# Optimization experiments

Measured on AMD Instinct MI355X. Metric: run time of the kernel, lower is better.

## Reference

```python
import jax, jax.numpy as jnp
import numpy as np

# dims: B=1, T=2048 (prefill), dim=3072, Hq=32, Hkv=8, D=128, S=max_seq_len=4096

def _rotate_interleave(x):
    # (-x1, x0, -x3, x2, ...) pairwise rotation on last dim
    x = x.reshape(x.shape[:-1] + (-1, 2))
    x = jnp.stack((-x[..., 1], x[..., 0]), axis=-1)
    return x.reshape(x.shape[:-2] + (-1,))


def setup_inputs() -> dict:
    key = jax.random.key(0)
    ks = jax.random.split(key, 8)
    B, T, DIM, HQ, HKV, HD, S = 1, 2048, 3072, 32, 8, 128, 4096
    x = jax.random.normal(ks[0], (B, T, DIM), jnp.float32)
    wq = jax.random.normal(ks[1], (HQ * HD, DIM), jnp.float32) * 0.02
    wk = jax.random.normal(ks[2], (HKV * HD, DIM), jnp.float32) * 0.02
    wv = jax.random.normal(ks[3], (HKV * HD, DIM), jnp.float32) * 0.02
    wo = jax.random.normal(ks[4], (DIM, HQ * HD), jnp.float32) * 0.02
    freqs_cos = jax.random.uniform(ks[5], (T, HD), jnp.float32)
    freqs_sin = jax.random.uniform(ks[6], (T, HD), jnp.float32)
    input_pos = jnp.zeros((1,), jnp.int32)
    k_cache = jnp.zeros((1, S, HKV, HD), jnp.float32)
    v_cache = jnp.zeros((1, S, HKV, HD), jnp.float32)
    return {"x": x, "wq": wq, "wk": wk, "wv": wv, "wo": wo,
            "freqs_cos": freqs_cos, "freqs_sin": freqs_sin,
            "k_cache": k_cache, "v_cache": v_cache, "input_pos": input_pos}


def reference(x, wq, wk, wv, wo, freqs_cos, freqs_sin, k_cache, v_cache, input_pos):
    B, T, _ = x.shape
    HQ, HKV, HD = 32, 8, 128
    q = (x @ wq.T).reshape(B, T, HQ, HD)
    k = (x @ wk.T).reshape(B, T, HKV, HD)
    v = (x @ wv.T).reshape(B, T, HKV, HD)
    # interleaved RoPE (computed in fp32 as in apply_rotary_emb)
    fc = freqs_cos[None, :, None, :]
    fs = freqs_sin[None, :, None, :]
    q = q * fc + _rotate_interleave(q) * fs
    k = k * fc + _rotate_interleave(k) * fs
    # KV-cache update at start_pos (torch.ops.llama.update_cache)
    sp = input_pos[0]
    k_all = jax.lax.dynamic_update_slice(k_cache, k, (0, sp, 0, 0))  # [1,S,HKV,HD]
    v_all = jax.lax.dynamic_update_slice(v_cache, v, (0, sp, 0, 0))
    S = k_all.shape[1]
    # GQA: expand kv heads to match q heads (head h -> kv head h // rep)
    rep = HQ // HKV
    kr = jnp.repeat(k_all, rep, axis=2)  # [1,S,HQ,HD]
    vr = jnp.repeat(v_all, rep, axis=2)
    scale = 1.0 / np.sqrt(HD).astype(np.float32)
    scores = jnp.einsum('bthd,bshd->bhts', q, kr) * scale  # [B,HQ,T,S]
    # causal mask relative to start_pos (custom_sdpa is_causal=True path)
    qpos = sp + jnp.arange(T)
    kpos = jnp.arange(S)
    mask = kpos[None, :] <= qpos[:, None]                   # [T,S]
    scores = jnp.where(mask[None, None], scores, jnp.float32(-1e30))
    attn = jax.nn.softmax(scores, axis=-1)
    y = jnp.einsum('bhts,bshd->bthd', attn, vr).reshape(B, T, HQ * HD)
    return y @ wo.T
```

## Files before the change

kernel.cpp:

```cpp
#include <hip/hip_runtime.h>
#include <hip/hip_bf16.h>
#include <stdint.h>

typedef float f32x4 __attribute__((ext_vector_type(4)));
typedef short s16x8 __attribute__((ext_vector_type(8)));
typedef short s16x4 __attribute__((ext_vector_type(4)));
typedef unsigned short u16x2 __attribute__((ext_vector_type(2)));
typedef unsigned short u16x4 __attribute__((ext_vector_type(4)));

#define AS1 __attribute__((address_space(1)))
#define AS3 __attribute__((address_space(3)))

static constexpr int T_    = 2048;
static constexpr int DIM_  = 3072;
static constexpr int HQ_   = 32;
static constexpr int HKV_  = 8;
static constexpr int HD_   = 128;
static constexpr int S_    = 4096;
static constexpr int NQKV_ = HQ_ * HD_ + 2 * HKV_ * HD_;

__device__ __forceinline__ unsigned short f2b(float f) {
  return __builtin_bit_cast(unsigned short, __float2bfloat16(f));
}
__device__ __forceinline__ float b2f(unsigned short u) {
  return __bfloat162float(__builtin_bit_cast(__hip_bfloat16, u));
}
__device__ __forceinline__ float exp2a(float x) {
  float r; asm("v_exp_f32 %0, %1" : "=v"(r) : "v"(x)); return r;
}

__device__ __forceinline__ void gld_lds16(const void* g, void* l) {
  __builtin_amdgcn_global_load_lds((AS1 unsigned int*)(uintptr_t)g,
                                   (AS3 unsigned int*)l, 16, 0, 0);
}

#define FENCE() asm volatile("" ::: "memory")
#define BAR()   do { FENCE(); __builtin_amdgcn_s_barrier(); FENCE(); } while (0)
#define WAIT_VM(n)   asm volatile("s_waitcnt vmcnt(" #n ")" ::: "memory")
#define WAIT_LGKM(n) asm volatile("s_waitcnt lgkmcnt(" #n ")" ::: "memory")
#define SCHEDB()     __builtin_amdgcn_sched_barrier(0)

__global__ __launch_bounds__(256)
void k_cvt(const float* __restrict__ src, unsigned short* __restrict__ dst, int n4) {
  int i = blockIdx.x * 256 + threadIdx.x;
  if (i >= n4) return;
  float4 v = reinterpret_cast<const float4*>(src)[i];
  u16x4 o;
  o.x = f2b(v.x); o.y = f2b(v.y); o.z = f2b(v.z); o.w = f2b(v.w);
  reinterpret_cast<u16x4*>(dst)[i] = o;
}

__global__ __launch_bounds__(256)
void k_cvtW(const float* __restrict__ wq, const float* __restrict__ wk,
            const float* __restrict__ wv, unsigned short* __restrict__ dst) {
  int idx = blockIdx.x * 256 + threadIdx.x;
  if (idx >= 4718592) return;
  const float* src; int s;
  if (idx < 3145728)      { src = wq; s = idx; }
  else if (idx < 3932160) { src = wk; s = idx - 3145728; }
  else                    { src = wv; s = idx - 3932160; }
  float4 v = reinterpret_cast<const float4*>(src)[s];
  u16x4 o;
  o.x = f2b(v.x); o.y = f2b(v.y); o.z = f2b(v.z); o.w = f2b(v.w);
  reinterpret_cast<u16x4*>(dst)[idx] = o;
}

template<bool OUT_BF16>
__global__ __launch_bounds__(512, 4)
void k_gemm192(const unsigned short* __restrict__ A,
               const unsigned short* __restrict__ B,
               void* __restrict__ Cout, int N, int K, int KT,
               int nbn, int xcdq) {
  __shared__ char lds[81920];
  const int bid = blockIdx.x;
  const int swz = (bid & 7) * xcdq + (bid >> 3);
  const int bm  = swz / nbn, bn = swz % nbn;
  const int tid = threadIdx.x, lane = tid & 63, wid = tid >> 6;
  const int wm  = wid >> 2, wn = wid & 3;
  const int r16 = lane & 15, q4 = lane >> 4;

  const unsigned short* Ag = A + (size_t)(bm * 128) * K;
  const unsigned short* Bg = B + (size_t)(bn * 192) * K;

  const int srow = tid >> 3;
  const int scol = ((tid & 7) ^ (srow & 7)) * 8;

  f32x4 acc[4][3] = {};
  s16x8 af[4][2];

  auto stageA = [&](int c, int r, int t) {
    gld_lds16(Ag + (size_t)(r * 64 + srow) * K + t * 64 + scol,
              lds + c * 40960 + r * 8192 + tid * 16);
  };
  auto stageB = [&](int c, int r, int t) {
    gld_lds16(Bg + (size_t)(r * 64 + srow) * K + t * 64 + scol,
              lds + c * 40960 + 16384 + r * 8192 + tid * 16);
  };
  auto readA = [&](int c) {
    #pragma unroll
    for (int i = 0; i < 4; ++i) {
      const int arow = wm * 64 + i * 16 + r16;
      #pragma unroll
      for (int kk = 0; kk < 2; ++kk)
        af[i][kk] = *(const s16x8*)(lds + c * 40960 + arow * 128 +
                                    (((kk * 4 + q4) ^ (arow & 7)) << 4));
    }
  };
  auto readB = [&](s16x8 (&dst)[2], int c, int j) {
    const int brow = wn * 48 + j * 16 + r16;
    #pragma unroll
    for (int kk = 0; kk < 2; ++kk)
      dst[kk] = *(const s16x8*)(lds + c * 40960 + 16384 + brow * 128 +
                                (((kk * 4 + q4) ^ (brow & 7)) << 4));
  };

#define MFMA8(BF, J)                                                           \
  __builtin_amdgcn_s_setprio(1);                                               \
  _Pragma("unroll")                                                            \
  for (int i_ = 0; i_ < 4; ++i_) {                                             \
    _Pragma("unroll")                                                          \
    for (int kk_ = 0; kk_ < 2; ++kk_)                                          \
      acc[i_][J] = __builtin_amdgcn_mfma_f32_16x16x32_bf16(                    \
          af[i_][kk_], BF[kk_], acc[i_][J], 0, 0, 0);                          \
  }                                                                            \
  __builtin_amdgcn_s_setprio(0);

  stageA(0, 0, 0); stageA(0, 1, 0);
  stageB(0, 0, 0); stageB(0, 1, 0); stageB(0, 2, 0);
  WAIT_VM(0);
  BAR();

  for (int t = 0; t < KT; ++t) {
    const int c = t & 1;
    const bool hn = (t + 1 < KT);
    {
      s16x8 bfc[2];
      readA(c); readB(bfc, c, 0);
      if (hn) { stageA(c ^ 1, 0, t + 1); stageA(c ^ 1, 1, t + 1); }
      BAR();
      WAIT_LGKM(0); SCHEDB();
      MFMA8(bfc, 0);
      BAR();
    }
    {
      s16x8 bfc[2];
      readB(bfc, c, 1);
      if (hn) { stageB(c ^ 1, 0, t + 1); stageB(c ^ 1, 1, t + 1); }
      BAR();
      WAIT_LGKM(0); SCHEDB();
      MFMA8(bfc, 1);
      BAR();
    }
    {
      s16x8 bfc[2];
      readB(bfc, c, 2);
      if (hn) stageB(c ^ 1, 2, t + 1);
      BAR();
      WAIT_LGKM(0); SCHEDB();
      MFMA8(bfc, 2);
      if (hn) { WAIT_VM(0); }
      BAR();
    }
  }
#undef MFMA8

  #pragma unroll
  for (int i = 0; i < 4; ++i) {
    const int row = bm * 128 + wm * 64 + i * 16 + q4 * 4;
    #pragma unroll
    for (int j = 0; j < 3; ++j) {
      const int col = bn * 192 + wn * 48 + j * 16 + r16;
      if constexpr (OUT_BF16) {
        unsigned short* C = (unsigned short*)Cout;
        #pragma unroll
        for (int rr = 0; rr < 4; ++rr)
          C[(size_t)(row + rr) * N + col] = f2b(acc[i][j][rr]);
      } else {
        float* C = (float*)Cout;
        #pragma unroll
        for (int rr = 0; rr < 4; ++rr)
          C[(size_t)(row + rr) * N + col] = acc[i][j][rr];
      }
    }
  }
}

__global__ __launch_bounds__(256)
void k_rope_q(const unsigned short* __restrict__ qkv,
              const float* __restrict__ fc, const float* __restrict__ fs,
              unsigned short* __restrict__ Qr) {
  int idx = blockIdx.x * 256 + threadIdx.x;
  int t   = idx >> 11;
  int rem = idx & 2047;
  int h   = rem >> 6;
  int d0  = (rem & 63) << 1;
  size_t qoff = (size_t)t * NQKV_ + h * HD_ + d0;
  u16x2 xv = *reinterpret_cast<const u16x2*>(&qkv[qoff]);
  float x0 = b2f(xv.x), x1 = b2f(xv.y);
  float c0 = fc[t * HD_ + d0], c1 = fc[t * HD_ + d0 + 1];
  float s0 = fs[t * HD_ + d0], s1 = fs[t * HD_ + d0 + 1];
  u16x2 o;
  o.x = f2b(x0 * c0 - x1 * s0);
  o.y = f2b(x1 * c1 + x0 * s1);
  *reinterpret_cast<u16x2*>(&Qr[((size_t)h * T_ + t) * HD_ + d0]) = o;
}

__global__ __launch_bounds__(256)
void k_rope_k(const unsigned short* __restrict__ qkv,
              const float* __restrict__ fc, const float* __restrict__ fs,
              unsigned short* __restrict__ Kall, const int* __restrict__ ipos) {
  int idx = blockIdx.x * 256 + threadIdx.x;
  int t   = idx >> 9;
  int rem = idx & 511;
  int hk  = rem >> 6;
  int d0  = (rem & 63) << 1;
  int sp  = ipos[0];
  size_t qoff = (size_t)t * NQKV_ + HQ_ * HD_ + hk * HD_ + d0;
  u16x2 xv = *reinterpret_cast<const u16x2*>(&qkv[qoff]);
  float x0 = b2f(xv.x), x1 = b2f(xv.y);
  float c0 = fc[t * HD_ + d0], c1 = fc[t * HD_ + d0 + 1];
  float s0 = fs[t * HD_ + d0], s1 = fs[t * HD_ + d0 + 1];
  unsigned short o0 = f2b(x0 * c0 - x1 * s0);
  unsigned short o1 = f2b(x1 * c1 + x0 * s1);
  size_t ooff = ((size_t)hk * S_ + sp + t) * HD_ + d0;
  Kall[ooff] = o0; Kall[ooff + 1] = o1;
}

__global__ __launch_bounds__(256)
void k_prefix(const float* __restrict__ kc, const float* __restrict__ vc,
              unsigned short* __restrict__ Kall, unsigned short* __restrict__ VT,
              const int* __restrict__ ipos) {
  int sp = ipos[0];
  int total = sp * HKV_ * HD_;
  for (int idx = blockIdx.x * 256 + threadIdx.x; idx < total;
       idx += gridDim.x * 256) {
    int s   = idx >> 10;
    int rem = idx & 1023;
    int hk  = rem >> 7;
    int d   = rem & 127;
    Kall[((size_t)hk * S_ + s) * HD_ + d] = f2b(kc[((size_t)s * HKV_ + hk) * HD_ + d]);
    VT[((size_t)hk * HD_ + d) * S_ + s]   = f2b(vc[((size_t)s * HKV_ + hk) * HD_ + d]);
  }
}

__global__ __launch_bounds__(256)
void k_vt(const unsigned short* __restrict__ qkv,
          unsigned short* __restrict__ VT, const int* __restrict__ ipos) {
  int hk = blockIdx.x >> 5;
  int tt = blockIdx.x & 31;
  int sp = ipos[0];
  __shared__ unsigned short lds[64][136];
  int tid = threadIdx.x;
  #pragma unroll
  for (int p = 0; p < 4; ++p) {
    int e   = p * 256 + tid;
    int tr  = e >> 4;
    int col = (e & 15) << 3;
    *reinterpret_cast<s16x8*>(&lds[tr][col]) =
        *reinterpret_cast<const s16x8*>(&qkv[(size_t)(tt * 64 + tr) * NQKV_ + (HQ_ + HKV_) * HD_ + hk * HD_ + col]);
  }
  __syncthreads();
  #pragma unroll
  for (int p = 0; p < 32; ++p) {
    int e = p * 256 + tid;
    int d = e >> 6;
    int t = e & 63;
    VT[((size_t)hk * HD_ + d) * S_ + sp + tt * 64 + t] = lds[t][d];
  }
}

__global__ __launch_bounds__(256, 2)
void k_attn(const unsigned short* __restrict__ Qr,
            const unsigned short* __restrict__ Kall,
            const unsigned short* __restrict__ VT,
            unsigned short* __restrict__ Y,
            const int* __restrict__ ipos) {
  constexpr int QB = 64, KB = 64;
  __shared__ char lds[65536];
  const int bid  = blockIdx.x;
  const int hk   = bid & 7;
  const int j2   = bid >> 3;
  const int h    = hk * 4 + (j2 & 3);
  const int qt   = 31 - (j2 >> 2);
  const int tid  = threadIdx.x, lane = tid & 63, wave = tid >> 6;
  const int r16  = lane & 15, q4 = lane >> 4;
  const int vx   = r16 & 7;
  const float NEG_INF = -__builtin_inff();
  const float MINIT   = -1.0e30f;

  const int sp = ipos[0];
  const int qbase = qt * QB + wave * 16;
  const unsigned short* Kbase = Kall + (size_t)hk * S_ * HD_;
  const unsigned short* Vbase = VT + (size_t)hk * HD_ * S_;

  s16x8 qf[4];
  const unsigned short* qp = Qr + ((size_t)h * T_ + qbase + r16) * HD_;
  #pragma unroll
  for (int ki = 0; ki < 4; ++ki)
    qf[ki] = *reinterpret_cast<const s16x8*>(qp + ki * 32 + q4 * 8);
  SCHEDB(); WAIT_VM(0); SCHEDB();

  auto stage = [&](int c, int jt) {
    #pragma unroll
    for (int p = 0; p < 4; ++p) {
      int e  = p * 256 + tid;
      int kr = e >> 4;
      int ks = (e & 15) ^ (kr & 7);
      gld_lds16(Kbase + (size_t)(jt * KB + kr) * HD_ + ks * 8,
                lds + c * 16384 + e * 16);
    }
    #pragma unroll
    for (int p = 0; p < 4; ++p) {
      int e  = p * 256 + tid;
      int vd = e >> 3;
      int vs = (e & 7) ^ (vd & 7);
      gld_lds16(Vbase + (size_t)vd * S_ + jt * KB + vs * 8,
                lds + 32768 + c * 16384 + e * 16);
    }
  };

  f32x4 o[8] = {};
  float m = MINIT, l = 0.f;
  const int qpos = sp + qbase + r16;
  const int qpos_wave_max = sp + qbase + 15;
  int jmax = (sp + qt * QB + QB - 1) >> 6;
  if (jmax > S_ / KB - 1) jmax = S_ / KB - 1;
  const float scale2 = 0.12751744416312068f;

  stage(0, 0);

  for (int j = 0; j <= jmax; ++j) {
    const int c = j & 1;
    if (j < jmax) { stage(c ^ 1, j + 1); WAIT_VM(8); }
    else         { WAIT_VM(0); }
    BAR();

    const bool active = (j * KB <= qpos_wave_max);
    if (active) {
      const char* kb = lds + c * 16384;
      const char* vb = lds + 32768 + c * 16384;
      f32x4 sfr[4];
      #pragma unroll
      for (int fn = 0; fn < 4; ++fn) {
        sfr[fn] = f32x4{0.f, 0.f, 0.f, 0.f};
        #pragma unroll
        for (int ki = 0; ki < 4; ++ki) {
          s16x8 kf = *(const s16x8*)(kb + (fn * 16 + r16) * 256 +
                                     (((ki * 4 + q4) ^ vx) << 4));
          sfr[fn] = __builtin_amdgcn_mfma_f32_16x16x32_bf16(kf, qf[ki], sfr[fn], 0, 0, 0);
        }
      }
      float p[16];
      const bool needMask = (j * KB + KB - 1) > (sp + qbase);
      if (needMask) {
        const int kbp = j * KB + q4 * 4;
        #pragma unroll
        for (int fn = 0; fn < 4; ++fn)
          #pragma unroll
          for (int r = 0; r < 4; ++r)
            p[fn * 4 + r] = (kbp + fn * 16 + r <= qpos) ? sfr[fn][r] * scale2 : NEG_INF;
      } else {
        #pragma unroll
        for (int fn = 0; fn < 4; ++fn)
          #pragma unroll
          for (int r = 0; r < 4; ++r)
            p[fn * 4 + r] = sfr[fn][r] * scale2;
      }
      float pmax = p[0];
      #pragma unroll
      for (int i = 1; i < 16; ++i) pmax = fmaxf(pmax, p[i]);
      pmax = fmaxf(pmax, __shfl_xor(pmax, 16));
      pmax = fmaxf(pmax, __shfl_xor(pmax, 32));
      if (!__all(pmax <= m + 8.0f)) {
        float mn = fmaxf(m, pmax);
        float alpha = exp2a(m - mn);
        m = mn; l *= alpha;
        #pragma unroll
        for (int r = 0; r < 4; ++r) {
          float aq = __shfl(alpha, q4 * 4 + r);
          #pragma unroll
          for (int db = 0; db < 8; ++db) o[db][r] *= aq;
        }
      }
      float rs = 0.f;
      #pragma unroll
      for (int i = 0; i < 16; ++i) { p[i] = exp2a(p[i] - m); rs += p[i]; }
      rs += __shfl_xor(rs, 16); rs += __shfl_xor(rs, 32);
      l += rs;
      s16x8 pf[2];
      #pragma unroll
      for (int w = 0; w < 2; ++w)
        #pragma unroll
        for (int i = 0; i < 8; ++i)
          pf[w][i] = (short)f2b(p[w * 8 + i]);
      const int voff = (q4 & 1) * 8;
      const int sbase = q4 >> 1;
      #pragma unroll
      for (int w = 0; w < 2; ++w) {
        #pragma unroll
        for (int db = 0; db < 8; ++db) {
          const char* vr = vb + (db * 16 + r16) * 128 + voff;
          s16x4 va = *(const s16x4*)(vr + (((w * 4 + sbase) ^ vx) << 4));
          s16x4 vb2 = *(const s16x4*)(vr + (((w * 4 + 2 + sbase) ^ vx) << 4));
          s16x8 vf = __builtin_shufflevector(va, vb2, 0, 1, 2, 3, 4, 5, 6, 7);
          o[db] = __builtin_amdgcn_mfma_f32_16x16x32_bf16(pf[w], vf, o[db], 0, 0, 0);
        }
      }
    }
    BAR();
  }

  float rcpl = 1.0f / l;
  float rlq[4];
  #pragma unroll
  for (int r = 0; r < 4; ++r) rlq[r] = __shfl(rcpl, q4 * 4 + r);
  #pragma unroll
  for (int db = 0; db < 8; ++db)
    #pragma unroll
    for (int r = 0; r < 4; ++r) {
      int t = qt * QB + wave * 16 + q4 * 4 + r;
      int d = db * 16 + r16;
      Y[(size_t)t * (HQ_ * HD_) + h * HD_ + d] = f2b(o[db][r] * rlq[r]);
    }
}

extern "C" void kernel_launch(void* const* d_in, const int* in_sizes, int n_in,
                              void* d_out, int out_size, void* d_ws, size_t ws_size,
                              hipStream_t stream) {
  const float* x  = (const float*)d_in[0];
  const float* wq = (const float*)d_in[1];
  const float* wk = (const float*)d_in[2];
  const float* wv = (const float*)d_in[3];
  const float* wo = (const float*)d_in[4];
  const float* fc = (const float*)d_in[5];
  const float* fs = (const float*)d_in[6];
  const float* kc = (const float*)d_in[7];
  const float* vc = (const float*)d_in[8];
  const int* ipos = (const int*)d_in[9];

  char* ws = (char*)d_ws;
  unsigned short* xb   = (unsigned short*)(ws);
  unsigned short* wqkv = (unsigned short*)(ws + 12582912);
  unsigned short* qkv  = (unsigned short*)(ws + 50331648);
  unsigned short* Qr   = (unsigned short*)(ws + 75497472);
  unsigned short* Kall = (unsigned short*)(ws + 92274688);
  unsigned short* VT   = (unsigned short*)(ws + 100663296);
  unsigned short* wo_b = (unsigned short*)(ws);
  unsigned short* y    = qkv;

  k_cvt<<<6144, 256, 0, stream>>>(x, xb, 6291456 / 4);
  k_cvtW<<<18432, 256, 0, stream>>>(wq, wk, wv, wqkv);

  k_gemm192<true><<<512, 512, 0, stream>>>(xb, wqkv, qkv, NQKV_, DIM_, 48, 32, 64);

  k_cvt<<<12288, 256, 0, stream>>>(wo, wo_b, 12582912 / 4);

  k_rope_q<<<16384, 256, 0, stream>>>(qkv, fc, fs, Qr);
  k_rope_k<<<4096, 256, 0, stream>>>(qkv, fc, fs, Kall, ipos);
  k_prefix<<<2048, 256, 0, stream>>>(kc, vc, Kall, VT, ipos);
  k_vt<<<256, 256, 0, stream>>>(qkv, VT, ipos);

  k_attn<<<1024, 256, 0, stream>>>(Qr, Kall, VT, y, ipos);

  k_gemm192<false><<<256, 512, 0, stream>>>(y, wo_b, d_out, DIM_, HQ_ * HD_, 64, 16, 32);
}
```

Baseline: 273.9 us.

## Fuse RoPE/cache prep kernels and use 64-row tiles for output GEMM

Merges the four post-QKV preparation kernels (Q RoPE, K RoPE, prefix cache copy, V transpose) into one launch partitioned by block index, and vectorizes RoPE to 8 elements per thread with float4 frequency loads. Templates the GEMM on the M tile size and runs the output projection with 64-row tiles, doubling its grid to fill more CUs. This cuts launch overhead and narrow memory accesses, but smaller tiles lower per-block reuse of the weight tile.

```diff
diff --git a/kernel.cpp b/kernel.cpp
--- a/kernel.cpp
+++ b/kernel.cpp
@@ -65,13 +65,16 @@
   reinterpret_cast<u16x4*>(dst)[idx] = o;
 }
 
-template<bool OUT_BF16>
+template<int BMT, bool OUT_BF16>
 __global__ __launch_bounds__(512, 4)
 void k_gemm192(const unsigned short* __restrict__ A,
                const unsigned short* __restrict__ B,
                void* __restrict__ Cout, int N, int K, int KT,
                int nbn, int xcdq) {
-  __shared__ char lds[81920];
+  constexpr int AROWS  = BMT / 64;
+  constexpr int AFRAG  = BMT / 32;
+  constexpr int LDSBUF = BMT * 128 + 24576;
+  __shared__ char lds[2 * LDSBUF];
   const int bid = blockIdx.x;
   const int swz = (bid & 7) * xcdq + (bid >> 3);
   const int bm  = swz / nbn, bn = swz % nbn;
@@ -79,30 +82,30 @@
   const int wm  = wid >> 2, wn = wid & 3;
   const int r16 = lane & 15, q4 = lane >> 4;
 
-  const unsigned short* Ag = A + (size_t)(bm * 128) * K;
+  const unsigned short* Ag = A + (size_t)(bm * BMT) * K;
   const unsigned short* Bg = B + (size_t)(bn * 192) * K;
 
   const int srow = tid >> 3;
   const int scol = ((tid & 7) ^ (srow & 7)) * 8;
 
-  f32x4 acc[4][3] = {};
-  s16x8 af[4][2];
+  f32x4 acc[AFRAG][3] = {};
+  s16x8 af[AFRAG][2];
 
   auto stageA = [&](int c, int r, int t) {
     gld_lds16(Ag + (size_t)(r * 64 + srow) * K + t * 64 + scol,
-              lds + c * 40960 + r * 8192 + tid * 16);
+              lds + c * LDSBUF + r * 8192 + tid * 16);
   };
   auto stageB = [&](int c, int r, int t) {
     gld_lds16(Bg + (size_t)(r * 64 + srow) * K + t * 64 + scol,
-              lds + c * 40960 + 16384 + r * 8192 + tid * 16);
+              lds + c * LDSBUF + BMT * 128 + r * 8192 + tid * 16);
   };
   auto readA = [&](int c) {
     #pragma unroll
-    for (int i = 0; i < 4; ++i) {
-      const int arow = wm * 64 + i * 16 + r16;
+    for (int i = 0; i < AFRAG; ++i) {
+      const int arow = wm * (BMT / 2) + i * 16 + r16;
       #pragma unroll
       for (int kk = 0; kk < 2; ++kk)
-        af[i][kk] = *(const s16x8*)(lds + c * 40960 + arow * 128 +
+        af[i][kk] = *(const s16x8*)(lds + c * LDSBUF + arow * 128 +
                                     (((kk * 4 + q4) ^ (arow & 7)) << 4));
     }
   };
@@ -110,14 +113,14 @@
     const int brow = wn * 48 + j * 16 + r16;
     #pragma unroll
     for (int kk = 0; kk < 2; ++kk)
-      dst[kk] = *(const s16x8*)(lds + c * 40960 + 16384 + brow * 128 +
+      dst[kk] = *(const s16x8*)(lds + c * LDSBUF + BMT * 128 + brow * 128 +
                                 (((kk * 4 + q4) ^ (brow & 7)) << 4));
   };
 
 #define MFMA8(BF, J)                                                           \
   __builtin_amdgcn_s_setprio(1);                                               \
   _Pragma("unroll")                                                            \
-  for (int i_ = 0; i_ < 4; ++i_) {                                             \
+  for (int i_ = 0; i_ < AFRAG; ++i_) {                                         \
     _Pragma("unroll")                                                          \
     for (int kk_ = 0; kk_ < 2; ++kk_)                                          \
       acc[i_][J] = __builtin_amdgcn_mfma_f32_16x16x32_bf16(                    \
@@ -125,7 +128,8 @@
   }                                                                            \
   __builtin_amdgcn_s_setprio(0);
 
-  stageA(0, 0, 0); stageA(0, 1, 0);
+  #pragma unroll
+  for (int r = 0; r < AROWS; ++r) stageA(0, r, 0);
   stageB(0, 0, 0); stageB(0, 1, 0); stageB(0, 2, 0);
   WAIT_VM(0);
   BAR();
@@ -136,7 +140,11 @@
     {
       s16x8 bfc[2];
       readA(c); readB(bfc, c, 0);
-      if (hn) { stageA(c ^ 1, 0, t + 1); stageA(c ^ 1, 1, t + 1); }
+      if (hn) {
+        stageA(c ^ 1, 0, t + 1);
+        if constexpr (BMT == 128) stageA(c ^ 1, 1, t + 1);
+        else                      stageB(c ^ 1, 0, t + 1);
+      }
       BAR();
       WAIT_LGKM(0); SCHEDB();
       MFMA8(bfc, 0);
@@ -145,7 +153,10 @@
     {
       s16x8 bfc[2];
       readB(bfc, c, 1);
-      if (hn) { stageB(c ^ 1, 0, t + 1); stageB(c ^ 1, 1, t + 1); }
+      if (hn) {
+        if constexpr (BMT == 128) { stageB(c ^ 1, 0, t + 1); stageB(c ^ 1, 1, t + 1); }
+        else                      { stageB(c ^ 1, 1, t + 1); }
+      }
       BAR();
       WAIT_LGKM(0); SCHEDB();
       MFMA8(bfc, 1);
@@ -165,8 +176,8 @@
 #undef MFMA8
 
   #pragma unroll
-  for (int i = 0; i < 4; ++i) {
-    const int row = bm * 128 + wm * 64 + i * 16 + q4 * 4;
+  for (int i = 0; i < AFRAG; ++i) {
+    const int row = bm * BMT + wm * (BMT / 2) + i * 16 + q4 * 4;
     #pragma unroll
     for (int j = 0; j < 3; ++j) {
       const int col = bn * 192 + wn * 48 + j * 16 + r16;
@@ -186,86 +197,95 @@
 }
 
 __global__ __launch_bounds__(256)
-void k_rope_q(const unsigned short* __restrict__ qkv,
-              const float* __restrict__ fc, const float* __restrict__ fs,
-              unsigned short* __restrict__ Qr) {
-  int idx = blockIdx.x * 256 + threadIdx.x;
-  int t   = idx >> 11;
-  int rem = idx & 2047;
-  int h   = rem >> 6;
-  int d0  = (rem & 63) << 1;
-  size_t qoff = (size_t)t * NQKV_ + h * HD_ + d0;
-  u16x2 xv = *reinterpret_cast<const u16x2*>(&qkv[qoff]);
-  float x0 = b2f(xv.x), x1 = b2f(xv.y);
-  float c0 = fc[t * HD_ + d0], c1 = fc[t * HD_ + d0 + 1];
-  float s0 = fs[t * HD_ + d0], s1 = fs[t * HD_ + d0 + 1];
-  u16x2 o;
-  o.x = f2b(x0 * c0 - x1 * s0);
-  o.y = f2b(x1 * c1 + x0 * s1);
-  *reinterpret_cast<u16x2*>(&Qr[((size_t)h * T_ + t) * HD_ + d0]) = o;
-}
-
-__global__ __launch_bounds__(256)
-void k_rope_k(const unsigned short* __restrict__ qkv,
-              const float* __restrict__ fc, const float* __restrict__ fs,
-              unsigned short* __restrict__ Kall, const int* __restrict__ ipos) {
-  int idx = blockIdx.x * 256 + threadIdx.x;
-  int t   = idx >> 9;
-  int rem = idx & 511;
-  int hk  = rem >> 6;
-  int d0  = (rem & 63) << 1;
-  int sp  = ipos[0];
-  size_t qoff = (size_t)t * NQKV_ + HQ_ * HD_ + hk * HD_ + d0;
-  u16x2 xv = *reinterpret_cast<const u16x2*>(&qkv[qoff]);
-  float x0 = b2f(xv.x), x1 = b2f(xv.y);
-  float c0 = fc[t * HD_ + d0], c1 = fc[t * HD_ + d0 + 1];
-  float s0 = fs[t * HD_ + d0], s1 = fs[t * HD_ + d0 + 1];
-  unsigned short o0 = f2b(x0 * c0 - x1 * s0);
-  unsigned short o1 = f2b(x1 * c1 + x0 * s1);
-  size_t ooff = ((size_t)hk * S_ + sp + t) * HD_ + d0;
-  Kall[ooff] = o0; Kall[ooff + 1] = o1;
-}
-
-__global__ __launch_bounds__(256)
-void k_prefix(const float* __restrict__ kc, const float* __restrict__ vc,
-              unsigned short* __restrict__ Kall, unsigned short* __restrict__ VT,
-              const int* __restrict__ ipos) {
-  int sp = ipos[0];
-  int total = sp * HKV_ * HD_;
-  for (int idx = blockIdx.x * 256 + threadIdx.x; idx < total;
-       idx += gridDim.x * 256) {
-    int s   = idx >> 10;
-    int rem = idx & 1023;
-    int hk  = rem >> 7;
-    int d   = rem & 127;
-    Kall[((size_t)hk * S_ + s) * HD_ + d] = f2b(kc[((size_t)s * HKV_ + hk) * HD_ + d]);
-    VT[((size_t)hk * HD_ + d) * S_ + s]   = f2b(vc[((size_t)s * HKV_ + hk) * HD_ + d]);
-  }
-}
-
-__global__ __launch_bounds__(256)
-void k_vt(const unsigned short* __restrict__ qkv,
-          unsigned short* __restrict__ VT, const int* __restrict__ ipos) {
-  int hk = blockIdx.x >> 5;
-  int tt = blockIdx.x & 31;
-  int sp = ipos[0];
+void k_prep(const unsigned short* __restrict__ qkv,
+            const float* __restrict__ fc, const float* __restrict__ fs,
+            const float* __restrict__ kc, const float* __restrict__ vc,
+            unsigned short* __restrict__ Qr, unsigned short* __restrict__ Kall,
+            unsigned short* __restrict__ VT, const int* __restrict__ ipos) {
   __shared__ unsigned short lds[64][136];
-  int tid = threadIdx.x;
-  #pragma unroll
-  for (int p = 0; p < 4; ++p) {
-    int e   = p * 256 + tid;
-    int tr  = e >> 4;
-    int col = (e & 15) << 3;
-    *reinterpret_cast<s16x8*>(&lds[tr][col]) =
-        *reinterpret_cast<const s16x8*>(&qkv[(size_t)(tt * 64 + tr) * NQKV_ + (HQ_ + HKV_) * HD_ + hk * HD_ + col]);
-  }
-  __syncthreads();
-  #pragma unroll
-  for (int p = 0; p < 32; ++p) {
-    int e = p * 256 + tid;
-    int d = e >> 6;
-    int t = e & 63;
-    VT[((size_t)hk * HD_ + d) * S_ + sp + tt * 64 + t] = lds[t][d];
+  const int b = blockIdx.x, tid = threadIdx.x;
+
+  if (b < 4096) {
+    int idx = b * 256 + tid;
+    int t   = idx >> 9;
+    int rem = idx & 511;
+    int h   = rem >> 4;
+    int c8  = (rem & 15) << 3;
+    s16x8 xv = *(const s16x8*)(qkv + (size_t)t * NQKV_ + h * HD_ + c8);
+    float4 ca = *(const float4*)(fc + t * HD_ + c8);
+    float4 cb = *(const float4*)(fc + t * HD_ + c8 + 4);
+    float4 sa = *(const float4*)(fs + t * HD_ + c8);
+    float4 sb = *(const float4*)(fs + t * HD_ + c8 + 4);
+    float cc[8] = {ca.x, ca.y, ca.z, ca.w, cb.x, cb.y, cb.z, cb.w};
+    float ss[8] = {sa.x, sa.y, sa.z, sa.w, sb.x, sb.y, sb.z, sb.w};
+    s16x8 o;
+    #pragma unroll
+    for (int i = 0; i < 4; ++i) {
+      float x0 = b2f((unsigned short)xv[2 * i]);
+      float x1 = b2f((unsigned short)xv[2 * i + 1]);
+      o[2 * i]     = (short)f2b(x0 * cc[2 * i]     - x1 * ss[2 * i]);
+      o[2 * i + 1] = (short)f2b(x1 * cc[2 * i + 1] + x0 * ss[2 * i + 1]);
+    }
+    *(s16x8*)(Qr + ((size_t)h * T_ + t) * HD_ + c8) = o;
+
+  } else if (b < 5120) {
+    int idx = (b - 4096) * 256 + tid;
+    int t   = idx >> 7;
+    int rem = idx & 127;
+    int hk  = rem >> 4;
+    int c8  = (rem & 15) << 3;
+    int sp  = ipos[0];
+    s16x8 xv = *(const s16x8*)(qkv + (size_t)t * NQKV_ + HQ_ * HD_ + hk * HD_ + c8);
+    float4 ca = *(const float4*)(fc + t * HD_ + c8);
+    float4 cb = *(const float4*)(fc + t * HD_ + c8 + 4);
+    float4 sa = *(const float4*)(fs + t * HD_ + c8);
+    float4 sb = *(const float4*)(fs + t * HD_ + c8 + 4);
+    float cc[8] = {ca.x, ca.y, ca.z, ca.w, cb.x, cb.y, cb.z, cb.w};
+    float ss[8] = {sa.x, sa.y, sa.z, sa.w, sb.x, sb.y, sb.z, sb.w};
+    s16x8 o;
+    #pragma unroll
+    for (int i = 0; i < 4; ++i) {
+      float x0 = b2f((unsigned short)xv[2 * i]);
+      float x1 = b2f((unsigned short)xv[2 * i + 1]);
+      o[2 * i]     = (short)f2b(x0 * cc[2 * i]     - x1 * ss[2 * i]);
+      o[2 * i + 1] = (short)f2b(x1 * cc[2 * i + 1] + x0 * ss[2 * i + 1]);
+    }
+    *(s16x8*)(Kall + ((size_t)hk * S_ + sp + t) * HD_ + c8) = o;
+
+  } else if (b < 5376) {
+    int bb = b - 5120;
+    int hk = bb >> 5;
+    int tt = bb & 31;
+    int sp = ipos[0];
+    #pragma unroll
+    for (int p = 0; p < 4; ++p) {
+      int e   = p * 256 + tid;
+      int tr  = e >> 4;
+      int col = (e & 15) << 3;
+      *reinterpret_cast<s16x8*>(&lds[tr][col]) =
+          *reinterpret_cast<const s16x8*>(&qkv[(size_t)(tt * 64 + tr) * NQKV_ +
+                                               (HQ_ + HKV_) * HD_ + hk * HD_ + col]);
+    }
+    __syncthreads();
+    #pragma unroll
+    for (int p = 0; p < 32; ++p) {
+      int e = p * 256 + tid;
+      int d = e >> 6;
+      int t = e & 63;
+      VT[((size_t)hk * HD_ + d) * S_ + sp + tt * 64 + t] = lds[t][d];
+    }
+
+  } else {
+    int sp = ipos[0];
+    int total = sp * HKV_ * HD_;
+    for (int idx = (b - 5376) * 256 + tid; idx < total; idx += 256 * 256) {
+      int s   = idx >> 10;
+      int rem = idx & 1023;
+      int hk  = rem >> 7;
+      int d   = rem & 127;
+      Kall[((size_t)hk * S_ + s) * HD_ + d] = f2b(kc[((size_t)s * HKV_ + hk) * HD_ + d]);
+      VT[((size_t)hk * HD_ + d) * S_ + s]   = f2b(vc[((size_t)s * HKV_ + hk) * HD_ + d]);
+    }
   }
 }
 
@@ -451,16 +471,13 @@
   k_cvt<<<6144, 256, 0, stream>>>(x, xb, 6291456 / 4);
   k_cvtW<<<18432, 256, 0, stream>>>(wq, wk, wv, wqkv);
 
-  k_gemm192<true><<<512, 512, 0, stream>>>(xb, wqkv, qkv, NQKV_, DIM_, 48, 32, 64);
+  k_gemm192<128, true><<<512, 512, 0, stream>>>(xb, wqkv, qkv, NQKV_, DIM_, 48, 32, 64);
 
   k_cvt<<<12288, 256, 0, stream>>>(wo, wo_b, 12582912 / 4);
 
-  k_rope_q<<<16384, 256, 0, stream>>>(qkv, fc, fs, Qr);
-  k_rope_k<<<4096, 256, 0, stream>>>(qkv, fc, fs, Kall, ipos);
-  k_prefix<<<2048, 256, 0, stream>>>(kc, vc, Kall, VT, ipos);
-  k_vt<<<256, 256, 0, stream>>>(qkv, VT, ipos);
+  k_prep<<<5632, 256, 0, stream>>>(qkv, fc, fs, kc, vc, Qr, Kall, VT, ipos);
 
   k_attn<<<1024, 256, 0, stream>>>(Qr, Kall, VT, y, ipos);
 
-  k_gemm192<false><<<256, 512, 0, stream>>>(y, wo_b, d_out, DIM_, HQ_ * HD_, 64, 16, 32);
-}
+  k_gemm192<64, false><<<512, 512, 0, stream>>>(y, wo_b, d_out, DIM_, HQ_ * HD_, 64, 16, 64);
+}
```

New measurement: 256.0 us. -6.5%, faster.
